# Performance work log

Measured on AMD Instinct MI355X. Metric: run time of the kernel, lower is better.

Reference implementation:

```python
import jax, jax.numpy as jnp
import numpy as np
from math import sqrt

POOL = 8  # pool_size from init_kwargs


def setup_inputs() -> dict:
    key = jax.random.key(0)
    k1, k2, k3 = jax.random.split(key, 3)
    b, c, h, w = 16, 64, 256, 256
    dim_k = 64
    x = jax.random.normal(k1, (b, c, h, w), dtype=jnp.float32)
    # torch nn.Linear(num_feat, dim_k, bias=False) weight: (dim_k, num_feat)
    bound = 1.0 / sqrt(c)
    Wq = jax.random.uniform(k2, (dim_k, c), minval=-bound, maxval=bound, dtype=jnp.float32)
    Wk = jax.random.uniform(k3, (dim_k, c), minval=-bound, maxval=bound, dtype=jnp.float32)
    return {"x": x, "Wq": Wq, "Wk": Wk}


def reference(x, Wq, Wk):
    p = POOL
    b, c, h, w = x.shape
    wh, ww = h // p, w // p  # window size
    n = p * p                # number of windows / pooled tokens
    dim_k = Wq.shape[0]
    scale = 1.0 / sqrt(dim_k)

    # AdaptiveAvgPool2d(p) with divisible dims == mean over (wh, ww) blocks
    y = x.reshape(b, c, p, wh, p, ww).mean(axis=(3, 5))  # (b, c, p, p)
    y = y.reshape(b, c, n).transpose(0, 2, 1)            # (b, n, c)

    q = jnp.einsum('bnc,kc->bnk', y, Wq)  # (b, n, dim_k)
    k = jnp.einsum('bnc,kc->bnk', y, Wk)  # (b, n, dim_k)

    # window_partition of x.permute(0,2,3,1) with window [wh, ww]
    xp = x.transpose(0, 2, 3, 1)                               # (b, h, w, c)
    v = xp.reshape(b, p, wh, p, ww, c)
    v = v.transpose(0, 1, 3, 2, 4, 5).reshape(b, n, wh * ww * c)  # (b, n, wh*ww*c)

    dist = jax.nn.softmax(jnp.einsum('bnk,bmk->bnm', q, k) * scale, axis=-1)  # (b, n, n)
    att = jnp.einsum('bnm,bmd->bnd', dist, v)  # (b, n, wh*ww*c)

    # window_reverse -> (b, h, w, c), then permute to (b, c, h, w)
    out = att.reshape(b, p, p, wh, ww, c)
    out = out.transpose(0, 1, 3, 2, 4, 5).reshape(b, h, w, c)
    return out.transpose(0, 3, 1, 2)
```

## Files before the change

### kernel.cpp

```cpp
#include <hip/hip_runtime.h>
#include <math.h>


typedef float nfloat4 __attribute__((ext_vector_type(4)));

__global__ __launch_bounds__(256) void pool_kernel(const float* __restrict__ x,
                                                   float* __restrict__ yT)
{
    int bc = blockIdx.x;
    int b  = bc >> 6, c = bc & 63;
    const float4* plane = (const float4*)(x + (size_t)bc * 65536);
    int t    = threadIdx.x;
    int col4 = t & 63;
    int q    = t >> 6;

    float acc[8];
#pragma unroll
    for (int wr = 0; wr < 8; ++wr) acc[wr] = 0.f;

#pragma unroll
    for (int wr = 0; wr < 8; ++wr) {
#pragma unroll
        for (int it = 0; it < 8; ++it) {
            int row = wr * 32 + it * 4 + q;
            float4 v = plane[row * 64 + col4];
            acc[wr] += v.x + v.y + v.z + v.w;
        }
    }

    __shared__ float red[8][264];
#pragma unroll
    for (int wr = 0; wr < 8; ++wr) red[wr][t] = acc[wr];
    __syncthreads();

    if (t < 64) {
        int wr = t >> 3, wc = t & 7;
        float s = 0.f;
#pragma unroll
        for (int qq = 0; qq < 4; ++qq)
#pragma unroll
            for (int ss = 0; ss < 8; ++ss)
                s += red[wr][qq * 64 + wc * 8 + ss];
        yT[b * 4096 + c * 64 + t] = s * (1.0f / 1024.0f);
    }
}

#define ST 68
__global__ __launch_bounds__(256) void attn_kernel(const float* __restrict__ yT,
                                                   const float* __restrict__ Wq,
                                                   const float* __restrict__ Wk,
                                                   float* __restrict__ distT)
{
    __shared__ float ylT[64 * ST];
    __shared__ float wqT[64 * ST];
    __shared__ float wkT[64 * ST];
    __shared__ float qlT[64 * ST];
    __shared__ float klT[64 * ST];
    __shared__ float sT [64 * ST];
    int b = blockIdx.x, t = threadIdx.x;

#pragma unroll
    for (int o = 0; o < 16; ++o) {
        int idx = o * 256 + t;
        int r = idx >> 6, cl = idx & 63;
        ylT[r * ST + cl] = yT[b * 4096 + idx];
        wqT[cl * ST + r] = Wq[idx];
        wkT[cl * ST + r] = Wk[idx];
    }
    __syncthreads();

    int lane = t & 63, ng = t >> 6;

    float qa[16], ka[16];
#pragma unroll
    for (int i = 0; i < 16; ++i) { qa[i] = 0.f; ka[i] = 0.f; }
    for (int c = 0; c < 64; ++c) {
        float wq = wqT[c * ST + lane];
        float wk = wkT[c * ST + lane];
        const float4* yr = (const float4*)(ylT + c * ST + ng * 16);
        float4 y0 = yr[0], y1 = yr[1], y2 = yr[2], y3 = yr[3];
        qa[0]  += y0.x * wq; qa[1]  += y0.y * wq; qa[2]  += y0.z * wq; qa[3]  += y0.w * wq;
        qa[4]  += y1.x * wq; qa[5]  += y1.y * wq; qa[6]  += y1.z * wq; qa[7]  += y1.w * wq;
        qa[8]  += y2.x * wq; qa[9]  += y2.y * wq; qa[10] += y2.z * wq; qa[11] += y2.w * wq;
        qa[12] += y3.x * wq; qa[13] += y3.y * wq; qa[14] += y3.z * wq; qa[15] += y3.w * wq;
        ka[0]  += y0.x * wk; ka[1]  += y0.y * wk; ka[2]  += y0.z * wk; ka[3]  += y0.w * wk;
        ka[4]  += y1.x * wk; ka[5]  += y1.y * wk; ka[6]  += y1.z * wk; ka[7]  += y1.w * wk;
        ka[8]  += y2.x * wk; ka[9]  += y2.y * wk; ka[10] += y2.z * wk; ka[11] += y2.w * wk;
        ka[12] += y3.x * wk; ka[13] += y3.y * wk; ka[14] += y3.z * wk; ka[15] += y3.w * wk;
    }
    {
        float4* qd = (float4*)(qlT + lane * ST + ng * 16);
        float4* kd = (float4*)(klT + lane * ST + ng * 16);
        qd[0] = make_float4(qa[0],  qa[1],  qa[2],  qa[3]);
        qd[1] = make_float4(qa[4],  qa[5],  qa[6],  qa[7]);
        qd[2] = make_float4(qa[8],  qa[9],  qa[10], qa[11]);
        qd[3] = make_float4(qa[12], qa[13], qa[14], qa[15]);
        kd[0] = make_float4(ka[0],  ka[1],  ka[2],  ka[3]);
        kd[1] = make_float4(ka[4],  ka[5],  ka[6],  ka[7]);
        kd[2] = make_float4(ka[8],  ka[9],  ka[10], ka[11]);
        kd[3] = make_float4(ka[12], ka[13], ka[14], ka[15]);
    }
    __syncthreads();

    float s[16];
#pragma unroll
    for (int i = 0; i < 16; ++i) s[i] = 0.f;
    for (int d = 0; d < 64; ++d) {
        float kv = klT[d * ST + lane];
        const float4* qr = (const float4*)(qlT + d * ST + ng * 16);
        float4 q0 = qr[0], q1 = qr[1], q2 = qr[2], q3 = qr[3];
        s[0]  += q0.x * kv; s[1]  += q0.y * kv; s[2]  += q0.z * kv; s[3]  += q0.w * kv;
        s[4]  += q1.x * kv; s[5]  += q1.y * kv; s[6]  += q1.z * kv; s[7]  += q1.w * kv;
        s[8]  += q2.x * kv; s[9]  += q2.y * kv; s[10] += q2.z * kv; s[11] += q2.w * kv;
        s[12] += q3.x * kv; s[13] += q3.y * kv; s[14] += q3.z * kv; s[15] += q3.w * kv;
    }
    const float scale = 0.125f;
#pragma unroll
    for (int i = 0; i < 16; ++i) {
        float v = s[i] * scale;
        float mx = v;
        mx = fmaxf(mx, __shfl_xor(mx, 1));
        mx = fmaxf(mx, __shfl_xor(mx, 2));
        mx = fmaxf(mx, __shfl_xor(mx, 4));
        mx = fmaxf(mx, __shfl_xor(mx, 8));
        mx = fmaxf(mx, __shfl_xor(mx, 16));
        mx = fmaxf(mx, __shfl_xor(mx, 32));
        float e = expf(v - mx);
        float sm = e;
        sm += __shfl_xor(sm, 1);
        sm += __shfl_xor(sm, 2);
        sm += __shfl_xor(sm, 4);
        sm += __shfl_xor(sm, 8);
        sm += __shfl_xor(sm, 16);
        sm += __shfl_xor(sm, 32);
        s[i] = e / sm;
    }
    {
        float4* sd = (float4*)(sT + lane * ST + ng * 16);
        sd[0] = make_float4(s[0],  s[1],  s[2],  s[3]);
        sd[1] = make_float4(s[4],  s[5],  s[6],  s[7]);
        sd[2] = make_float4(s[8],  s[9],  s[10], s[11]);
        sd[3] = make_float4(s[12], s[13], s[14], s[15]);
    }
    __syncthreads();

#pragma unroll
    for (int o = 0; o < 16; ++o) {
        int idx = o * 256 + t;
        int m = idx >> 6, n = idx & 63;
        distT[b * 4096 + idx] = sT[m * ST + n];
    }
}

#define XL_ISTRIDE 2052
__global__ __launch_bounds__(256) void combine_kernel(const float* __restrict__ x,
                                                      const float* __restrict__ distT,
                                                      float* __restrict__ out)
{
    __shared__ float Xl[4 * XL_ISTRIDE];
    int blk = blockIdx.x;
    int ig  = blk & 7;
    int bc  = 1023 - (blk >> 3);
    int b   = bc >> 6;
    const float* plane  = x   + (size_t)bc * 65536;
    float*       oplane = out + (size_t)bc * 65536;
    int t = threadIdx.x;

    float4* Xl4 = (float4*)Xl;
    const float4* plane4 = (const float4*)plane;
#pragma unroll
    for (int o = 0; o < 8; ++o) {
        int f4        = o * 256 + t;
        int row_local = f4 >> 6;
        int col4      = f4 & 63;
        int i         = row_local >> 3;
        int m_row     = row_local & 7;
        int g_row     = m_row * 32 + ig * 4 + i;
        Xl4[i * (XL_ISTRIDE / 4) + m_row * 64 + col4] = plane4[g_row * 64 + col4];
    }
    __syncthreads();

    int j4 = t & 7;
    int i  = (t >> 3) & 3;
    int tg = t >> 5;
    const float4* Xr = (const float4*)Xl + i * (XL_ISTRIDE / 4) + j4;
    const float4* Dg = (const float4*)(distT + b * 4096) + tg * 2;

    float4 acc[8];
#pragma unroll
    for (int r = 0; r < 8; ++r) acc[r] = make_float4(0.f, 0.f, 0.f, 0.f);

#pragma unroll 8
    for (int m = 0; m < 64; ++m) {
        int m_row = m >> 3, m_col = m & 7;
        float4 v  = Xr[m_row * 64 + m_col * 8];
        float4 d0 = Dg[m * 16];
        float4 d1 = Dg[m * 16 + 1];
        acc[0].x += d0.x * v.x; acc[0].y += d0.x * v.y; acc[0].z += d0.x * v.z; acc[0].w += d0.x * v.w;
        acc[1].x += d0.y * v.x; acc[1].y += d0.y * v.y; acc[1].z += d0.y * v.z; acc[1].w += d0.y * v.w;
        acc[2].x += d0.z * v.x; acc[2].y += d0.z * v.y; acc[2].z += d0.z * v.z; acc[2].w += d0.z * v.w;
        acc[3].x += d0.w * v.x; acc[3].y += d0.w * v.y; acc[3].z += d0.w * v.z; acc[3].w += d0.w * v.w;
        acc[4].x += d1.x * v.x; acc[4].y += d1.x * v.y; acc[4].z += d1.x * v.z; acc[4].w += d1.x * v.w;
        acc[5].x += d1.y * v.x; acc[5].y += d1.y * v.y; acc[5].z += d1.y * v.z; acc[5].w += d1.y * v.w;
        acc[6].x += d1.z * v.x; acc[6].y += d1.z * v.y; acc[6].z += d1.z * v.z; acc[6].w += d1.z * v.w;
        acc[7].x += d1.w * v.x; acc[7].y += d1.w * v.y; acc[7].z += d1.w * v.z; acc[7].w += d1.w * v.w;
    }

    nfloat4* orow = (nfloat4*)((float*)(oplane + (tg * 32 + ig * 4 + i) * 256)) + j4;
#pragma unroll
    for (int r = 0; r < 8; ++r) {
        nfloat4 v;
        v.x = acc[r].x; v.y = acc[r].y; v.z = acc[r].z; v.w = acc[r].w;
        __builtin_nontemporal_store(v, &orow[r * 8]);
    }
}

extern "C" void kernel_launch(void* const* d_in, const int* in_sizes, int n_in,
                              void* d_out, int out_size, void* d_ws, size_t ws_size,
                              hipStream_t stream)
{
    const float* x  = (const float*)d_in[0];
    const float* Wq = (const float*)d_in[1];
    const float* Wk = (const float*)d_in[2];
    float* out = (float*)d_out;

    float* y_ws  = (float*)d_ws;
    float* distT = y_ws + 65536;

    pool_kernel   <<<1024, 256, 0, stream>>>(x, y_ws);
    attn_kernel   <<<16,   256, 0, stream>>>(y_ws, Wq, Wk, distT);
    combine_kernel<<<8192, 256, 0, stream>>>(x, distT, out);
}
```

Before: 557.7 us.

## Rewrite combine kernel to register-accumulate all 64 windows without shared memory

The combine kernel drops its shared-memory staging of x. Each thread now loads 8 x values per window-row group straight from global memory and accumulates all 64 output windows in registers, reading dist weights through uniform (scalar/broadcast) loads. The attention kernel writes dist in non-transposed layout directly from registers, removing a shared buffer and a barrier. The grid is halved to 4096 blocks. Per-thread register use rises sharply (64 accumulators), and stores become scalar and strided across 64 rows, which may hurt occupancy and coalescing.

```diff
diff --git a/kernel.cpp b/kernel.cpp
--- a/kernel.cpp
+++ b/kernel.cpp
@@ -49,14 +49,13 @@
 __global__ __launch_bounds__(256) void attn_kernel(const float* __restrict__ yT,
                                                    const float* __restrict__ Wq,
                                                    const float* __restrict__ Wk,
-                                                   float* __restrict__ distT)
+                                                   float* __restrict__ distN)
 {
     __shared__ float ylT[64 * ST];
     __shared__ float wqT[64 * ST];
     __shared__ float wkT[64 * ST];
     __shared__ float qlT[64 * ST];
     __shared__ float klT[64 * ST];
-    __shared__ float sT [64 * ST];
     int b = blockIdx.x, t = threadIdx.x;
 
 #pragma unroll
@@ -135,84 +134,50 @@
         sm += __shfl_xor(sm, 32);
         s[i] = e / sm;
     }
-    {
-        float4* sd = (float4*)(sT + lane * ST + ng * 16);
-        sd[0] = make_float4(s[0],  s[1],  s[2],  s[3]);
-        sd[1] = make_float4(s[4],  s[5],  s[6],  s[7]);
-        sd[2] = make_float4(s[8],  s[9],  s[10], s[11]);
-        sd[3] = make_float4(s[12], s[13], s[14], s[15]);
-    }
-    __syncthreads();
-
 #pragma unroll
-    for (int o = 0; o < 16; ++o) {
-        int idx = o * 256 + t;
-        int m = idx >> 6, n = idx & 63;
-        distT[b * 4096 + idx] = sT[m * ST + n];
-    }
+    for (int i = 0; i < 16; ++i)
+        distN[b * 4096 + (ng * 16 + i) * 64 + lane] = s[i];
 }
 
-#define XL_ISTRIDE 2052
-__global__ __launch_bounds__(256) void combine_kernel(const float* __restrict__ x,
-                                                      const float* __restrict__ distT,
-                                                      float* __restrict__ out)
+__global__ __launch_bounds__(256, 4) void combine_kernel(const float* __restrict__ x,
+                                                         const float* __restrict__ distN,
+                                                         float* __restrict__ out)
 {
-    __shared__ float Xl[4 * XL_ISTRIDE];
     int blk = blockIdx.x;
-    int ig  = blk & 7;
-    int bc  = 1023 - (blk >> 3);
+    int rg  = blk & 3;
+    int bc  = 1023 - (blk >> 2);
     int b   = bc >> 6;
     const float* plane  = x   + (size_t)bc * 65536;
     float*       oplane = out + (size_t)bc * 65536;
+    const float* D      = distN + b * 4096;
+
     int t = threadIdx.x;
+    int j = t & 31;
+    int i = rg * 8 + (t >> 5);
 
-    float4* Xl4 = (float4*)Xl;
-    const float4* plane4 = (const float4*)plane;
+    float acc[64];
 #pragma unroll
-    for (int o = 0; o < 8; ++o) {
-        int f4        = o * 256 + t;
-        int row_local = f4 >> 6;
-        int col4      = f4 & 63;
-        int i         = row_local >> 3;
-        int m_row     = row_local & 7;
-        int g_row     = m_row * 32 + ig * 4 + i;
-        Xl4[i * (XL_ISTRIDE / 4) + m_row * 64 + col4] = plane4[g_row * 64 + col4];
-    }
-    __syncthreads();
+    for (int n = 0; n < 64; ++n) acc[n] = 0.f;
 
-    int j4 = t & 7;
-    int i  = (t >> 3) & 3;
-    int tg = t >> 5;
-    const float4* Xr = (const float4*)Xl + i * (XL_ISTRIDE / 4) + j4;
-    const float4* Dg = (const float4*)(distT + b * 4096) + tg * 2;
-
-    float4 acc[8];
+    for (int mb = 0; mb < 8; ++mb) {
+        const float* xrow = plane + (mb * 32 + i) * 256 + j;
+        float xv[8];
 #pragma unroll
-    for (int r = 0; r < 8; ++r) acc[r] = make_float4(0.f, 0.f, 0.f, 0.f);
-
-#pragma unroll 8
-    for (int m = 0; m < 64; ++m) {
-        int m_row = m >> 3, m_col = m & 7;
-        float4 v  = Xr[m_row * 64 + m_col * 8];
-        float4 d0 = Dg[m * 16];
-        float4 d1 = Dg[m * 16 + 1];
-        acc[0].x += d0.x * v.x; acc[0].y += d0.x * v.y; acc[0].z += d0.x * v.z; acc[0].w += d0.x * v.w;
-        acc[1].x += d0.y * v.x; acc[1].y += d0.y * v.y; acc[1].z += d0.y * v.z; acc[1].w += d0.y * v.w;
-        acc[2].x += d0.z * v.x; acc[2].y += d0.z * v.y; acc[2].z += d0.z * v.z; acc[2].w += d0.z * v.w;
-        acc[3].x += d0.w * v.x; acc[3].y += d0.w * v.y; acc[3].z += d0.w * v.z; acc[3].w += d0.w * v.w;
-        acc[4].x += d1.x * v.x; acc[4].y += d1.x * v.y; acc[4].z += d1.x * v.z; acc[4].w += d1.x * v.w;
-        acc[5].x += d1.y * v.x; acc[5].y += d1.y * v.y; acc[5].z += d1.y * v.z; acc[5].w += d1.y * v.w;
-        acc[6].x += d1.z * v.x; acc[6].y += d1.z * v.y; acc[6].z += d1.z * v.z; acc[6].w += d1.z * v.w;
-        acc[7].x += d1.w * v.x; acc[7].y += d1.w * v.y; acc[7].z += d1.w * v.z; acc[7].w += d1.w * v.w;
+        for (int mm = 0; mm < 8; ++mm)
+            xv[mm] = xrow[mm * 32];
+        const float* Db = D + mb * 8;
+#pragma unroll
+        for (int n = 0; n < 64; ++n) {
+#pragma unroll
+            for (int mm = 0; mm < 8; ++mm)
+                acc[n] = fmaf(Db[n * 64 + mm], xv[mm], acc[n]);
+        }
     }
 
-    nfloat4* orow = (nfloat4*)((float*)(oplane + (tg * 32 + ig * 4 + i) * 256)) + j4;
+    float* obase = oplane + i * 256 + j;
 #pragma unroll
-    for (int r = 0; r < 8; ++r) {
-        nfloat4 v;
-        v.x = acc[r].x; v.y = acc[r].y; v.z = acc[r].z; v.w = acc[r].w;
-        __builtin_nontemporal_store(v, &orow[r * 8]);
-    }
+    for (int n = 0; n < 64; ++n)
+        __builtin_nontemporal_store(acc[n], obase + (n >> 3) * 8192 + (n & 7) * 32);
 }
 
 extern "C" void kernel_launch(void* const* d_in, const int* in_sizes, int n_in,
@@ -225,9 +190,9 @@
     float* out = (float*)d_out;
 
     float* y_ws  = (float*)d_ws;
-    float* distT = y_ws + 65536;
+    float* distN = y_ws + 65536;
 
     pool_kernel   <<<1024, 256, 0, stream>>>(x, y_ws);
-    attn_kernel   <<<16,   256, 0, stream>>>(y_ws, Wq, Wk, distT);
-    combine_kernel<<<8192, 256, 0, stream>>>(x, distT, out);
+    attn_kernel   <<<16,   256, 0, stream>>>(y_ws, Wq, Wk, distN);
+    combine_kernel<<<4096, 256, 0, stream>>>(x, distN, out);
 }
```

Result: slower. 785.1 us (+40.8%).
